# Optimization experiments

Hardware: AMD Instinct MI355X
Metric: run time of the kernel (lower is better)

Reference implementation:

```python
import jax, jax.numpy as jnp
import numpy as np

N = 100000   # nodes per node type ('net' and 'cell')
E = 600000   # edges per canonical relation
D_IN = 16    # raw input feature dim
D = 128      # hidden dim (in_size == out_size, required by wl: Linear(2*D -> D))
SLOPE = 0.2  # DGL GATConv leaky_relu negative slope


def setup_inputs() -> dict:
    key = jax.random.key(0)
    ks = jax.random.split(key, 24)
    f = lambda k, shp, scale=1.0: jax.random.normal(k, shp, dtype=jnp.float32) * scale
    s_in = 1.0 / np.sqrt(D_IN).astype(np.float32)
    s_d = 1.0 / np.sqrt(D).astype(np.float32)
    s_2d = 1.0 / np.sqrt(2 * D).astype(np.float32)
    inp = {
        'x_net':   f(ks[0], (N, D_IN)),
        'x_cell':  f(ks[1], (N, D_IN)),
        'Wp_net':  f(ks[2], (D, D_IN), s_in),
        'Wp_cell': f(ks[3], (D, D_IN), s_in),
        # per-edge-type GATConv params: fc weight + attn_l + attn_r (num_heads=1, no bias)
        'Wg0': f(ks[4], (D, D), s_d), 'al0': f(ks[5], (D,), s_d), 'ar0': f(ks[6], (D,), s_d),
        'Wg1': f(ks[7], (D, D), s_d), 'al1': f(ks[8], (D,), s_d), 'ar1': f(ks[9], (D,), s_d),
        'Wg2': f(ks[10], (D, D), s_d), 'al2': f(ks[11], (D,), s_d), 'ar2': f(ks[12], (D,), s_d),
        'Wl':   f(ks[13], (D, 2 * D), s_2d),
        'bias': jnp.zeros((D,), jnp.float32),
        # edge lists: relation 0 = cell->net, 1 = net->cell, 2 = net->net
        'src0': jax.random.randint(ks[14], (E,), 0, N, dtype=jnp.int32),
        'dst0': jax.random.randint(ks[15], (E,), 0, N, dtype=jnp.int32),
        'src1': jax.random.randint(ks[16], (E,), 0, N, dtype=jnp.int32),
        'dst1': jax.random.randint(ks[17], (E,), 0, N, dtype=jnp.int32),
        'src2': jax.random.randint(ks[18], (E,), 0, N, dtype=jnp.int32),
        'dst2': jax.random.randint(ks[19], (E,), 0, N, dtype=jnp.int32),
    }
    return inp


def _gat(x_src, x_dst, W, al, ar, src, dst):
    """DGL GATConv (num_heads=1, bias=False) on one relation's edge list."""
    h_src = x_src @ W.T                               # [N, D]
    h_dst = x_dst @ W.T                               # [N, D]
    el = (h_src @ al)[src]                            # [E] gathered src logits
    er = (h_dst @ ar)[dst]                            # [E] gathered dst logits
    e = jax.nn.leaky_relu(el + er, SLOPE)             # [E]
    # segment softmax over incoming edges of each dst node
    m = jax.ops.segment_max(e, dst, num_segments=N)
    ex = jnp.exp(e - m[dst])
    denom = jax.ops.segment_sum(ex, dst, num_segments=N)
    alpha = ex / denom[dst]                           # [E]
    return jax.ops.segment_sum(h_src[src] * alpha[:, None], dst, num_segments=N)


def reference(x_net, x_cell, Wp_net, Wp_cell,
              Wg0, al0, ar0, Wg1, al1, ar1, Wg2, al2, ar2,
              Wl, bias,
              src0, dst0, src1, dst1, src2, dst2):
    # feature projection per node type (ParaGraph.feat_proj)
    h_net = x_net @ Wp_net.T                          # [N, D]
    h_cell = x_cell @ Wp_cell.T                       # [N, D]
    feat = {'net': h_net, 'cell': h_cell}
    out = {'net': jnp.zeros((N, D), h_net.dtype), 'cell': jnp.zeros((N, D), h_cell.dtype)}
    # canonical etypes: (srctype, dsttype, gat params, edge list)
    rels = [
        ('cell', 'net', Wg0, al0, ar0, src0, dst0),
        ('net', 'cell', Wg1, al1, ar1, src1, dst1),
        ('net', 'net',  Wg2, al2, ar2, src2, dst2),
    ]
    for st, dt, W, al, ar, src, dst in rels:
        out[dt] = out[dt] + _gat(feat[st], feat[dt], W, al, ar, src, dst)
        # faithful to the original: concat+linear+relu recomputed for EVERY ntype
        # inside the etype loop (the redundant fused-op pattern)
        for nt in ('net', 'cell'):
            out[nt] = jax.nn.relu(
                jnp.concatenate([feat[nt], out[nt] + bias], axis=1) @ Wl.T)
    return jnp.stack([out['net'], out['cell']])      # [2, N, D]
```

## Files before the change

### kernel.cpp

```cpp
#include <hip/hip_runtime.h>
#include <hip/hip_bf16.h>
#include <stdint.h>

#define NN 100000
#define NE 600000
#define SP 136
#define NB 782
#define BCAP 1600
#define CHUNK 4096
#define NCH ((NE + CHUNK - 1) / CHUNK)

typedef unsigned short u16;
typedef unsigned int u32;
typedef __attribute__((ext_vector_type(8))) short short8;
typedef __attribute__((ext_vector_type(8))) __bf16 bf16x8;
typedef __attribute__((ext_vector_type(4))) float floatx4;

__device__ __forceinline__ float b2f(u16 u) {
  union { float f; u32 i; } c; c.i = ((u32)u) << 16; return c.f;
}
__device__ __forceinline__ u16 f2b(float f) {
  union { float f; u32 i; } c; c.f = f;
  u32 r = c.i + 0x7FFFu + ((c.i >> 16) & 1u);
  return (u16)(r >> 16);
}

__global__ __launch_bounds__(256) void conv_k(const float* __restrict__ Wl,
                                              const float* __restrict__ Wg0,
                                              const float* __restrict__ Wg1,
                                              const float* __restrict__ Wg2,
                                              u16* __restrict__ Wl_bf, u16* __restrict__ Wg_bf) {
  int y = blockIdx.y;
  const float* src = (y == 0) ? Wl : (y == 1) ? Wg0 : (y == 2) ? Wg1 : Wg2;
  u16* dst = (y == 0) ? Wl_bf : Wg_bf + (size_t)(y - 1) * 16384;
  int n = (y == 0) ? 32768 : 16384;
  int i = (blockIdx.x * 256 + threadIdx.x) * 4;
  if (i >= n) return;
  float4 v = *(const float4*)(src + i);
  ushort4 p; p.x = f2b(v.x); p.y = f2b(v.y); p.z = f2b(v.z); p.w = f2b(v.w);
  *(ushort4*)(dst + i) = p;
}

__global__ __launch_bounds__(256) void proj_k(const float* __restrict__ x_net, const float* __restrict__ x_cell,
                                              const float* __restrict__ Wp_net, const float* __restrict__ Wp_cell,
                                              u16* __restrict__ feat_net, u16* __restrict__ feat_cell) {
  const float* x  = blockIdx.y ? x_cell : x_net;
  const float* Wp = blockIdx.y ? Wp_cell : Wp_net;
  u16* feat       = blockIdx.y ? feat_cell : feat_net;
  __shared__ float Ws[128 * 17];
  __shared__ float xs[16][17];
  int tid = threadIdx.x;
#pragma unroll
  for (int it = 0; it < 8; ++it) {
    int idx = it * 256 + tid;
    int j = idx >> 4, k = idx & 15;
    Ws[j * 17 + k] = Wp[idx];
  }
  int n0 = blockIdx.x * 16;
  { int nn = tid >> 4, k = tid & 15;
    xs[nn][k] = x[(size_t)(n0 + nn) * 16 + k]; }
  __syncthreads();
  int j = tid & 127, g = tid >> 7;
  float acc[8];
#pragma unroll
  for (int r = 0; r < 8; ++r) acc[r] = 0.f;
#pragma unroll
  for (int k = 0; k < 16; ++k) {
    float w = Ws[j * 17 + k];
#pragma unroll
    for (int r = 0; r < 8; ++r) acc[r] += xs[g * 8 + r][k] * w;
  }
#pragma unroll
  for (int r = 0; r < 8; ++r)
    feat[(size_t)(n0 + g * 8 + r) * 128 + j] = f2b(acc[r]);
}

__global__ __launch_bounds__(128) void vec_k(const float* Wg0, const float* al0, const float* ar0,
                                             const float* Wg1, const float* al1, const float* ar1,
                                             const float* Wg2, const float* al2, const float* ar2,
                                             const float* Wl, const float* bias,
                                             float* __restrict__ vecs) {
  int a = blockIdx.x;
  int j = threadIdx.x;
  float s = 0.f;
  if (a < 6) {
    const float* W = (a < 2) ? Wg0 : (a < 4) ? Wg1 : Wg2;
    const float* v = (a == 0) ? al0 : (a == 1) ? ar0 : (a == 2) ? al1 : (a == 3) ? ar1 : (a == 4) ? al2 : ar2;
    for (int i = 0; i < 128; ++i) s += W[i * 128 + j] * v[i];
  } else {
    for (int i = 0; i < 128; ++i) s += Wl[(size_t)j * 256 + 128 + i] * bias[i];
  }
  vecs[a * 128 + j] = s;
}

__global__ __launch_bounds__(256) void logits_k(const u16* __restrict__ feat_net, const u16* __restrict__ feat_cell,
                                                const float* __restrict__ vecs, float* __restrict__ outs) {
  __shared__ float vs[6 * 128];
  int tid = threadIdx.x;
#pragma unroll
  for (int it = 0; it < 3; ++it) vs[it * 256 + tid] = vecs[it * 256 + tid];
  __syncthreads();
  int y = blockIdx.y;
  const u16* f = y ? feat_cell : feat_net;
  int n = blockIdx.x * 256 + tid;
  if (n >= NN) return;
  const u16* row = f + (size_t)n * 128;
  if (y == 0) {
    float s1 = 0.f, s2 = 0.f, s4 = 0.f, s5 = 0.f;
#pragma unroll
    for (int k = 0; k < 128; k += 8) {
      short8 u = *(const short8*)(row + k);
#pragma unroll
      for (int t = 0; t < 8; ++t) {
        float fv = b2f((u16)u[t]);
        s1 += fv * vs[1 * 128 + k + t]; s2 += fv * vs[2 * 128 + k + t];
        s4 += fv * vs[4 * 128 + k + t]; s5 += fv * vs[5 * 128 + k + t];
      }
    }
    outs[(size_t)1 * NN + n] = s1; outs[(size_t)2 * NN + n] = s2;
    outs[(size_t)4 * NN + n] = s4; outs[(size_t)5 * NN + n] = s5;
  } else {
    float s0 = 0.f, s3 = 0.f;
#pragma unroll
    for (int k = 0; k < 128; k += 8) {
      short8 u = *(const short8*)(row + k);
#pragma unroll
      for (int t = 0; t < 8; ++t) {
        float fv = b2f((u16)u[t]);
        s0 += fv * vs[0 * 128 + k + t]; s3 += fv * vs[3 * 128 + k + t];
      }
    }
    outs[(size_t)0 * NN + n] = s0; outs[(size_t)3 * NN + n] = s3;
  }
}

__global__ __launch_bounds__(256) void bhist_k(const int* __restrict__ dst0, const int* __restrict__ dst1,
                                               const int* __restrict__ dst2, int* __restrict__ bcnt) {
  int r = blockIdx.y;
  const int* dst = (r == 0) ? dst0 : (r == 1) ? dst1 : dst2;
  __shared__ int h[NB];
  int tid = threadIdx.x;
  for (int i = tid; i < NB; i += 256) h[i] = 0;
  __syncthreads();
  int e0 = blockIdx.x * CHUNK;
  int cnt = NE - e0; if (cnt > CHUNK) cnt = CHUNK;
  for (int i = tid; i < cnt; i += 256) atomicAdd(&h[((u32)dst[e0 + i]) >> 7], 1);
  __syncthreads();
  for (int b = tid; b < NB; b += 256) {
    int c = h[b];
    if (c) atomicAdd(&bcnt[(size_t)r * NB + b], c);
  }
}

__global__ __launch_bounds__(1024) void bscan_k(const int* __restrict__ bcnt, int* __restrict__ bptr,
                                                int* __restrict__ bcur) {
  int r = blockIdx.x, t = threadIdx.x;
  const int* c = bcnt + (size_t)r * NB;
  int* p = bptr + (size_t)r * (NB + 1);
  int* cur = bcur + (size_t)r * NB;
  int v = (t < NB) ? c[t] : 0;
  __shared__ int ss[1024];
  ss[t] = v; __syncthreads();
  for (int off = 1; off < 1024; off <<= 1) {
    int u = (t >= off) ? ss[t - off] : 0;
    __syncthreads();
    ss[t] += u;
    __syncthreads();
  }
  if (t < NB) { int e = ss[t] - v; p[t] = e; cur[t] = e; }
  if (t == 1023) p[NB] = ss[1023];
}

__global__ __launch_bounds__(256) void bscatter_k(const int* __restrict__ src0, const int* __restrict__ dst0,
                                                  const int* __restrict__ src1, const int* __restrict__ dst1,
                                                  const int* __restrict__ src2, const int* __restrict__ dst2,
                                                  int* __restrict__ bcur, u32* __restrict__ recs) {
  int r = blockIdx.y;
  const int* src = (r == 0) ? src0 : (r == 1) ? src1 : src2;
  const int* dst = (r == 0) ? dst0 : (r == 1) ? dst1 : dst2;
  __shared__ int hist[NB];
  __shared__ int lstart[NB];
  __shared__ int lcur[NB];
  __shared__ int badj[NB];
  __shared__ u32 rbuf[CHUNK];
  __shared__ u16 kbuf[CHUNK];
  __shared__ int ss[256];
  int tid = threadIdx.x;
  int e0 = blockIdx.x * CHUNK;
  int cnt = NE - e0; if (cnt > CHUNK) cnt = CHUNK;

  for (int i = tid; i < NB; i += 256) hist[i] = 0;
  __syncthreads();
  for (int i = tid; i < cnt; i += 256) atomicAdd(&hist[((u32)dst[e0 + i]) >> 7], 1);
  __syncthreads();
  int loc[4]; int s = 0;
  int base4 = tid * 4;
#pragma unroll
  for (int j = 0; j < 4; ++j) {
    int idx = base4 + j;
    int v = (idx < NB) ? hist[idx] : 0;
    loc[j] = s; s += v;
  }
  ss[tid] = s; __syncthreads();
  for (int off = 1; off < 256; off <<= 1) {
    int u = (tid >= off) ? ss[tid - off] : 0;
    __syncthreads();
    ss[tid] += u;
    __syncthreads();
  }
  int ex = ss[tid] - s;
#pragma unroll
  for (int j = 0; j < 4; ++j) {
    int idx = base4 + j;
    if (idx < NB) { int e = ex + loc[j]; lstart[idx] = e; lcur[idx] = e; }
  }
  __syncthreads();
  for (int b = tid; b < NB; b += 256) {
    int c = hist[b];
    int g = 0;
    if (c) g = atomicAdd(&bcur[(size_t)r * NB + b], c);
    badj[b] = g - lstart[b];
  }
  __syncthreads();
  for (int i = tid; i < cnt; i += 256) {
    int dN = dst[e0 + i], sN = src[e0 + i];
    int b = ((u32)dN) >> 7;
    int pos = atomicAdd(&lcur[b], 1);
    rbuf[pos] = ((u32)(dN & 127) << 17) | (u32)sN;
    kbuf[pos] = (u16)b;
  }
  __syncthreads();
  u32* out = recs + (size_t)r * NE;
  for (int i = tid; i < cnt; i += 256) {
    int b = kbuf[i];
    out[badj[b] + i] = rbuf[i];
  }
}

__global__ __launch_bounds__(256) void sort_k(u32* __restrict__ recs, const int* __restrict__ bptr,
                                              int* __restrict__ rowptr) {
  int r = blockIdx.y, b = blockIdx.x, tid = threadIdx.x;
  const int* p = bptr + (size_t)r * (NB + 1);
  u32* rec = recs + (size_t)r * NE;
  int* rp = rowptr + (size_t)r * (NN + 1);
  int base = p[b], end = p[b + 1];
  int cnt = end - base; if (cnt > BCAP) cnt = BCAP;
  __shared__ u32 rs[BCAP];
  __shared__ int hist[128], excl[128], cur[128];
  for (int i = tid; i < cnt; i += 256) rs[i] = rec[base + i];
  if (tid < 128) hist[tid] = 0;
  __syncthreads();
  for (int i = tid; i < cnt; i += 256) atomicAdd(&hist[rs[i] >> 17], 1);
  __syncthreads();
  if (tid < 128) cur[tid] = hist[tid];
  __syncthreads();
  for (int off = 1; off < 128; off <<= 1) {
    int v = 0;
    if (tid < 128 && tid >= off) v = cur[tid - off];
    __syncthreads();
    if (tid < 128) cur[tid] += v;
    __syncthreads();
  }
  if (tid < 128) {
    int e = cur[tid] - hist[tid];
    excl[tid] = e;
    int node = b * 128 + tid;
    if (node < NN) rp[node] = base + e;
  }
  if (b == NB - 1 && tid == 0) rp[NN] = p[NB];
  if (tid < 128) cur[tid] = excl[tid];
  __syncthreads();
  for (int i = tid; i < cnt; i += 256) {
    u32 v = rs[i];
    int pos = atomicAdd(&cur[v >> 17], 1);
    rec[base + pos] = v & 0x1FFFFu;
  }
}

template<int RMW>
__global__ __launch_bounds__(256) void agg_k(const u16* __restrict__ h, const u32* __restrict__ srecs,
                                             const int* __restrict__ rp,
                                             const float* __restrict__ el, const float* __restrict__ er,
                                             u16* __restrict__ out) {
  int tid = threadIdx.x;
  int sub = tid & 15;
  int n = blockIdx.x * 16 + (tid >> 4);
  int start = rp[n], end = rp[n + 1];
  u16* orow = out + (size_t)n * 128 + sub * 8;
  if (start == end) {
    if (!RMW) *(short8*)orow = short8{0, 0, 0, 0, 0, 0, 0, 0};
    return;
  }
  float ern = er[n];
  float acc[8];
#pragma unroll
  for (int t = 0; t < 8; ++t) acc[t] = 0.f;
  float sl = 0.f;
  const u16* hsub = h + sub * 8;
  for (int base = start; base < end; base += 16) {
    int m = end - base; if (m > 16) m = 16;
    int srci = 0; float w = 0.f;
    if (sub < m) {
      srci = (int)srecs[base + sub];
      float l = el[srci] + ern;
      l = (l >= 0.f) ? l : 0.2f * l;
      w = __expf(l);
    }
    sl += w;
    for (int i = 0; i < m; ++i) {
      float x = __shfl(w, i, 16);
      int sv = __shfl(srci, i, 16);
      short8 hv = *(const short8*)(hsub + (size_t)sv * 128);
#pragma unroll
      for (int t = 0; t < 8; ++t) acc[t] += x * b2f((u16)hv[t]);
    }
  }
  float s = sl;
#pragma unroll
  for (int off = 8; off > 0; off >>= 1) s += __shfl_xor(s, off, 16);
  float inv = 1.f / s;
  short8 o;
  if (RMW) {
    short8 pv = *(const short8*)orow;
#pragma unroll
    for (int t = 0; t < 8; ++t) o[t] = (short)f2b(b2f((u16)pv[t]) + acc[t] * inv);
  } else {
#pragma unroll
    for (int t = 0; t < 8; ++t) o[t] = (short)f2b(acc[t] * inv);
  }
  *(short8*)orow = o;
}

struct BJob { const u16* A; const u16* W; int ldw; int woff; u16* C; };
struct BJobs5 { BJob j[5]; };
__global__ __launch_bounds__(256) void gemm_bf_k(BJobs5 jobs) {
  BJob jb = jobs.j[blockIdx.y];
  __shared__ u16 Wlds[128 * SP];
  const int tid = threadIdx.x;
  const int row0 = blockIdx.x * 64;
#pragma unroll
  for (int it = 0; it < 8; ++it) {
    int idx = it * 256 + tid;
    int r = idx >> 4, c = (idx & 15) << 3;
    *(short8*)(&Wlds[r * SP + c]) = *(const short8*)(jb.W + (size_t)r * jb.ldw + jb.woff + c);
  }
  const int lane = tid & 63, wv = tid >> 6;
  const int m16 = lane & 15, quad = lane >> 4;
  int arow = row0 + wv * 16 + m16;
  if (arow >= NN) arow = NN - 1;
  const u16* Ab = jb.A + (size_t)arow * 128 + quad * 8;
  bf16x8 a[4];
#pragma unroll
  for (int kk = 0; kk < 4; ++kk) a[kk] = *(const bf16x8*)(Ab + kk * 32);
  __syncthreads();
  const u16* brow = &Wlds[m16 * SP + quad * 8];
  floatx4 acc[8];
#pragma unroll
  for (int c = 0; c < 8; ++c) acc[c] = floatx4{0.f, 0.f, 0.f, 0.f};
#pragma unroll
  for (int kk = 0; kk < 4; ++kk) {
#pragma unroll
    for (int c = 0; c < 8; ++c) {
      bf16x8 bfr = *(const bf16x8*)(brow + c * 16 * SP + kk * 32);
      acc[c] = __builtin_amdgcn_mfma_f32_16x16x32_bf16(a[kk], bfr, acc[c], 0, 0, 0);
    }
  }
#pragma unroll
  for (int c = 0; c < 8; ++c) {
    int col = c * 16 + m16;
#pragma unroll
    for (int r = 0; r < 4; ++r) {
      int grow = row0 + wv * 16 + quad * 4 + r;
      if (grow < NN) jb.C[(size_t)grow * 128 + col] = f2b(acc[c][r]);
    }
  }
}

struct FJob { const u16* A; const u16* P; void* C; };
struct FJobs2 { FJob j[2]; const u16* W; const float* cvec; };
template<int FINAL>
__global__ __launch_bounds__(256) void fused_k(FJobs2 jobs) {
  FJob jb = jobs.j[blockIdx.y];
  __shared__ u16 Wlds[128 * SP];
  const int tid = threadIdx.x;
  const int row0 = blockIdx.x * 64;
#pragma unroll
  for (int it = 0; it < 8; ++it) {
    int idx = it * 256 + tid;
    int r = idx >> 4, c = (idx & 15) << 3;
    *(short8*)(&Wlds[r * SP + c]) = *(const short8*)(jobs.W + (size_t)r * 256 + c);
  }
  const int lane = tid & 63, wv = tid >> 6;
  const int m16 = lane & 15, quad = lane >> 4;
  int arow = row0 + wv * 16 + m16;
  if (arow >= NN) arow = NN - 1;
  const u16* Ab = jb.A + (size_t)arow * 128 + quad * 8;
  bf16x8 a[4];
#pragma unroll
  for (int kk = 0; kk < 4; ++kk) a[kk] = *(const bf16x8*)(Ab + kk * 32);
  __syncthreads();
  const u16* brow = &Wlds[m16 * SP + quad * 8];
  floatx4 acc[8];
#pragma unroll
  for (int c = 0; c < 8; ++c) acc[c] = floatx4{0.f, 0.f, 0.f, 0.f};
#pragma unroll
  for (int kk = 0; kk < 4; ++kk) {
#pragma unroll
    for (int c = 0; c < 8; ++c) {
      bf16x8 bfr = *(const bf16x8*)(brow + c * 16 * SP + kk * 32);
      acc[c] = __builtin_amdgcn_mfma_f32_16x16x32_bf16(a[kk], bfr, acc[c], 0, 0, 0);
    }
  }
#pragma unroll
  for (int c = 0; c < 8; ++c) {
    int col = c * 16 + m16;
    float cv = jobs.cvec[col];
#pragma unroll
    for (int r = 0; r < 4; ++r) {
      int grow = row0 + wv * 16 + quad * 4 + r;
      if (grow < NN) {
        float v = acc[c][r] + b2f(jb.P[(size_t)grow * 128 + col]) + cv;
        v = fmaxf(v, 0.f);
        if (FINAL) ((float*)jb.C)[(size_t)grow * 128 + col] = v;
        else       ((u16*)jb.C)[(size_t)grow * 128 + col] = f2b(v);
      }
    }
  }
}

__global__ __launch_bounds__(256) void elem_k(const u16* __restrict__ P, const float* __restrict__ vecs,
                                              u16* __restrict__ out) {
  __shared__ float cs[128];
  if (threadIdx.x < 128) cs[threadIdx.x] = vecs[6 * 128 + threadIdx.x];
  __syncthreads();
  size_t idx = ((size_t)blockIdx.x * 256 + threadIdx.x) * 8;
  if (idx >= (size_t)NN * 128) return;
  int col = (int)(idx & 127);
  short8 u = *(const short8*)(P + idx);
  short8 w;
#pragma unroll
  for (int t = 0; t < 8; ++t)
    w[t] = (short)f2b(fmaxf(b2f((u16)u[t]) + cs[col + t], 0.f));
  *(short8*)(out + idx) = w;
}

extern "C" void kernel_launch(void* const* d_in, const int* in_sizes, int n_in,
                              void* d_out, int out_size, void* d_ws, size_t ws_size,
                              hipStream_t stream) {
  const float* x_net   = (const float*)d_in[0];
  const float* x_cell  = (const float*)d_in[1];
  const float* Wp_net  = (const float*)d_in[2];
  const float* Wp_cell = (const float*)d_in[3];
  const float* Wg[3] = {(const float*)d_in[4], (const float*)d_in[7], (const float*)d_in[10]};
  const float* al[3] = {(const float*)d_in[5], (const float*)d_in[8], (const float*)d_in[11]};
  const float* ar[3] = {(const float*)d_in[6], (const float*)d_in[9], (const float*)d_in[12]};
  const float* Wl    = (const float*)d_in[13];
  const float* bias  = (const float*)d_in[14];
  const int* src[3] = {(const int*)d_in[15], (const int*)d_in[17], (const int*)d_in[19]};
  const int* dst[3] = {(const int*)d_in[16], (const int*)d_in[18], (const int*)d_in[20]};

  char* ws = (char*)d_ws;
  size_t off = 0;
  auto alloc = [&](size_t b) { void* p = ws + off; off = (off + b + 255) & ~(size_t)255; return p; };
  u16*  feat_net  = (u16*)alloc((size_t)NN * 128 * 2);
  u16*  feat_cell = (u16*)alloc((size_t)NN * 128 * 2);
  u16*  hbuf0     = (u16*)alloc((size_t)NN * 128 * 2);
  u16*  hbuf1     = (u16*)alloc((size_t)NN * 128 * 2);
  u16*  hbuf2     = (u16*)alloc((size_t)NN * 128 * 2);
  u16*  P_net     = (u16*)alloc((size_t)NN * 128 * 2);
  u16*  P_cell    = (u16*)alloc((size_t)NN * 128 * 2);
  u16*  buf_net   = (u16*)alloc((size_t)NN * 128 * 2);
  u16*  buf_cell  = (u16*)alloc((size_t)NN * 128 * 2);
  float* vecs     = (float*)alloc(7 * 128 * 4);
  float* logit    = (float*)alloc((size_t)6 * NN * 4);
  u16*   Wl_bf    = (u16*)alloc((size_t)128 * 256 * 2);
  u16*   Wg_bf    = (u16*)alloc((size_t)3 * 128 * 128 * 2);
  int*   bcnt     = (int*)alloc((size_t)3 * NB * 4);
  int*   bcur     = (int*)alloc((size_t)3 * NB * 4);
  int*   bptr     = (int*)alloc((size_t)3 * (NB + 1) * 4);
  int*   rowptr   = (int*)alloc((size_t)3 * (NN + 1) * 4);
  u32*   recs     = (u32*)alloc((size_t)3 * NE * 4);

  hipMemsetAsync(bcnt, 0, (size_t)3 * NB * 4, stream);

  conv_k<<<dim3(32, 4), 256, 0, stream>>>(Wl, Wg[0], Wg[1], Wg[2], Wl_bf, Wg_bf);
  proj_k<<<dim3(NN / 16, 2), 256, 0, stream>>>(x_net, x_cell, Wp_net, Wp_cell, feat_net, feat_cell);
  vec_k<<<7, 128, 0, stream>>>(Wg[0], al[0], ar[0], Wg[1], al[1], ar[1], Wg[2], al[2], ar[2], Wl, bias, vecs);
  logits_k<<<dim3((NN + 255) / 256, 2), 256, 0, stream>>>(feat_net, feat_cell, vecs, logit);

  bhist_k<<<dim3(NCH, 3), 256, 0, stream>>>(dst[0], dst[1], dst[2], bcnt);
  bscan_k<<<3, 1024, 0, stream>>>(bcnt, bptr, bcur);
  bscatter_k<<<dim3(NCH, 3), 256, 0, stream>>>(src[0], dst[0], src[1], dst[1], src[2], dst[2],
                                               bcur, recs);
  sort_k<<<dim3(NB, 3), 256, 0, stream>>>(recs, bptr, rowptr);

  const int gb = (NN + 63) / 64;
  {
    BJobs5 jobs;
    jobs.j[0] = {feat_net,  Wl_bf,          256, 0, P_net};
    jobs.j[1] = {feat_cell, Wl_bf,          256, 0, P_cell};
    jobs.j[2] = {feat_cell, Wg_bf,          128, 0, hbuf0};
    jobs.j[3] = {feat_net,  Wg_bf + 16384,  128, 0, hbuf1};
    jobs.j[4] = {feat_net,  Wg_bf + 32768,  128, 0, hbuf2};
    gemm_bf_k<<<dim3(gb, 5), 256, 0, stream>>>(jobs);
  }

  float* out_f = (float*)d_out;
  const int ab = NN / 16;

  agg_k<0><<<ab, 256, 0, stream>>>(hbuf0, recs, rowptr, logit, logit + (size_t)NN, buf_net);
  {
    FJobs2 jobs; jobs.W = Wl_bf + 128; jobs.cvec = vecs + 6 * 128;
    jobs.j[0] = {buf_net, P_net, buf_net}; jobs.j[1] = jobs.j[0];
    fused_k<0><<<dim3(gb, 1), 256, 0, stream>>>(jobs);
  }
  elem_k<<<(NN * 128 / 8 + 255) / 256, 256, 0, stream>>>(P_cell, vecs, buf_cell);

  agg_k<1><<<ab, 256, 0, stream>>>(hbuf1, recs + (size_t)NE, rowptr + (NN + 1),
                                   logit + (size_t)2 * NN, logit + (size_t)3 * NN, buf_cell);
  {
    FJobs2 jobs; jobs.W = Wl_bf + 128; jobs.cvec = vecs + 6 * 128;
    jobs.j[0] = {buf_net, P_net, buf_net};
    jobs.j[1] = {buf_cell, P_cell, buf_cell};
    fused_k<0><<<dim3(gb, 2), 256, 0, stream>>>(jobs);
  }

  agg_k<1><<<ab, 256, 0, stream>>>(hbuf2, recs + (size_t)2 * NE, rowptr + 2 * (NN + 1),
                                   logit + (size_t)4 * NN, logit + (size_t)5 * NN, buf_net);
  {
    FJobs2 jobs; jobs.W = Wl_bf + 128; jobs.cvec = vecs + 6 * 128;
    jobs.j[0] = {buf_net, P_net, out_f};
    jobs.j[1] = {buf_cell, P_cell, out_f + (size_t)NN * 128};
    fused_k<1><<<dim3(gb, 2), 256, 0, stream>>>(jobs);
  }
}
```

Measured before the change: 517.9 us.

## Merge independent kernels into combined launches and reorder the per-relation stages

Several small or independent kernels are merged into multi-role launches that branch on block index: weight conversion, projection, vector precompute and zeroing of the histogram counts in one kernel; logits plus the bucket histogram in another; the sort plus the batched GEMM; and each aggregation paired with an independent fused linear job. The final cell output is computed alongside the last aggregation instead of after it. This cuts launch count and the idle tails between dependent stages by letting unrelated work fill the GPU together. In exchange the merged kernels take the larger shared-memory footprint of the GEMM role, which can lower occupancy for the aggregation blocks.

```diff
diff --git a/kernel.cpp b/kernel.cpp
--- a/kernel.cpp
+++ b/kernel.cpp
@@ -8,7 +8,9 @@
 #define NB 782
 #define BCAP 1600
 #define CHUNK 4096
-#define NCH ((NE + CHUNK - 1) / CHUNK)
+#define NCH 147
+#define GB 1563
+#define AB 6250
 
 typedef unsigned short u16;
 typedef unsigned int u32;
@@ -25,130 +27,274 @@
   return (u16)(r >> 16);
 }
 
-__global__ __launch_bounds__(256) void conv_k(const float* __restrict__ Wl,
-                                              const float* __restrict__ Wg0,
-                                              const float* __restrict__ Wg1,
-                                              const float* __restrict__ Wg2,
-                                              u16* __restrict__ Wl_bf, u16* __restrict__ Wg_bf) {
-  int y = blockIdx.y;
-  const float* src = (y == 0) ? Wl : (y == 1) ? Wg0 : (y == 2) ? Wg1 : Wg2;
-  u16* dst = (y == 0) ? Wl_bf : Wg_bf + (size_t)(y - 1) * 16384;
-  int n = (y == 0) ? 32768 : 16384;
-  int i = (blockIdx.x * 256 + threadIdx.x) * 4;
-  if (i >= n) return;
-  float4 v = *(const float4*)(src + i);
-  ushort4 p; p.x = f2b(v.x); p.y = f2b(v.y); p.z = f2b(v.z); p.w = f2b(v.w);
-  *(ushort4*)(dst + i) = p;
-}
-
-__global__ __launch_bounds__(256) void proj_k(const float* __restrict__ x_net, const float* __restrict__ x_cell,
-                                              const float* __restrict__ Wp_net, const float* __restrict__ Wp_cell,
-                                              u16* __restrict__ feat_net, u16* __restrict__ feat_cell) {
-  const float* x  = blockIdx.y ? x_cell : x_net;
-  const float* Wp = blockIdx.y ? Wp_cell : Wp_net;
-  u16* feat       = blockIdx.y ? feat_cell : feat_net;
-  __shared__ float Ws[128 * 17];
-  __shared__ float xs[16][17];
-  int tid = threadIdx.x;
+
+__device__ __forceinline__ void gemm_w(const u16* __restrict__ W, int ldw, u16* __restrict__ C,
+                                       u16* lds, int tid, int row0, const bf16x8* a,
+                                       int m16, int quad, int wv) {
 #pragma unroll
   for (int it = 0; it < 8; ++it) {
     int idx = it * 256 + tid;
-    int j = idx >> 4, k = idx & 15;
-    Ws[j * 17 + k] = Wp[idx];
-  }
-  int n0 = blockIdx.x * 16;
-  { int nn = tid >> 4, k = tid & 15;
-    xs[nn][k] = x[(size_t)(n0 + nn) * 16 + k]; }
-  __syncthreads();
-  int j = tid & 127, g = tid >> 7;
+    int r = idx >> 4, c = (idx & 15) << 3;
+    *(short8*)(&lds[r * SP + c]) = *(const short8*)(W + (size_t)r * ldw + c);
+  }
+  __syncthreads();
+  const u16* brow = &lds[m16 * SP + quad * 8];
+  floatx4 acc[8];
+#pragma unroll
+  for (int c = 0; c < 8; ++c) acc[c] = floatx4{0.f, 0.f, 0.f, 0.f};
+#pragma unroll
+  for (int kk = 0; kk < 4; ++kk) {
+#pragma unroll
+    for (int c = 0; c < 8; ++c) {
+      bf16x8 bfr = *(const bf16x8*)(brow + c * 16 * SP + kk * 32);
+      acc[c] = __builtin_amdgcn_mfma_f32_16x16x32_bf16(a[kk], bfr, acc[c], 0, 0, 0);
+    }
+  }
+#pragma unroll
+  for (int c = 0; c < 8; ++c) {
+    int col = c * 16 + m16;
+#pragma unroll
+    for (int r = 0; r < 4; ++r) {
+      int grow = row0 + wv * 16 + quad * 4 + r;
+      if (grow < NN) C[(size_t)grow * 128 + col] = f2b(acc[c][r]);
+    }
+  }
+}
+
+template<int FINAL>
+__device__ __forceinline__ void fused_body(int blk, int tid, const u16* __restrict__ A,
+                                           const u16* __restrict__ P, void* __restrict__ C,
+                                           const u16* __restrict__ W, const float* __restrict__ cvec,
+                                           u16* Wlds) {
+  const int row0 = blk * 64;
+#pragma unroll
+  for (int it = 0; it < 8; ++it) {
+    int idx = it * 256 + tid;
+    int r = idx >> 4, c = (idx & 15) << 3;
+    *(short8*)(&Wlds[r * SP + c]) = *(const short8*)(W + (size_t)r * 256 + c);
+  }
+  const int lane = tid & 63, wv = tid >> 6;
+  const int m16 = lane & 15, quad = lane >> 4;
+  int arow = row0 + wv * 16 + m16;
+  if (arow >= NN) arow = NN - 1;
+  const u16* Ab = A + (size_t)arow * 128 + quad * 8;
+  bf16x8 a[4];
+#pragma unroll
+  for (int kk = 0; kk < 4; ++kk) a[kk] = *(const bf16x8*)(Ab + kk * 32);
+  __syncthreads();
+  const u16* brow = &Wlds[m16 * SP + quad * 8];
+  floatx4 acc[8];
+#pragma unroll
+  for (int c = 0; c < 8; ++c) acc[c] = floatx4{0.f, 0.f, 0.f, 0.f};
+#pragma unroll
+  for (int kk = 0; kk < 4; ++kk) {
+#pragma unroll
+    for (int c = 0; c < 8; ++c) {
+      bf16x8 bfr = *(const bf16x8*)(brow + c * 16 * SP + kk * 32);
+      acc[c] = __builtin_amdgcn_mfma_f32_16x16x32_bf16(a[kk], bfr, acc[c], 0, 0, 0);
+    }
+  }
+#pragma unroll
+  for (int c = 0; c < 8; ++c) {
+    int col = c * 16 + m16;
+    float cv = cvec[col];
+#pragma unroll
+    for (int r = 0; r < 4; ++r) {
+      int grow = row0 + wv * 16 + quad * 4 + r;
+      if (grow < NN) {
+        float v = acc[c][r] + b2f(P[(size_t)grow * 128 + col]) + cv;
+        v = fmaxf(v, 0.f);
+        if (FINAL) ((float*)C)[(size_t)grow * 128 + col] = v;
+        else       ((u16*)C)[(size_t)grow * 128 + col] = f2b(v);
+      }
+    }
+  }
+}
+
+template<int RMW>
+__device__ __forceinline__ void agg_body(int nb, int tid, const u16* __restrict__ h,
+                                         const u32* __restrict__ srecs, const int* __restrict__ rp,
+                                         const float* __restrict__ el, const float* __restrict__ er,
+                                         u16* __restrict__ out) {
+  int sub = tid & 15;
+  int n = nb * 16 + (tid >> 4);
+  int start = rp[n], end = rp[n + 1];
+  u16* orow = out + (size_t)n * 128 + sub * 8;
+  if (start == end) {
+    if (!RMW) *(short8*)orow = short8{0, 0, 0, 0, 0, 0, 0, 0};
+    return;
+  }
+  float ern = er[n];
   float acc[8];
 #pragma unroll
-  for (int r = 0; r < 8; ++r) acc[r] = 0.f;
-#pragma unroll
-  for (int k = 0; k < 16; ++k) {
-    float w = Ws[j * 17 + k];
-#pragma unroll
-    for (int r = 0; r < 8; ++r) acc[r] += xs[g * 8 + r][k] * w;
-  }
-#pragma unroll
-  for (int r = 0; r < 8; ++r)
-    feat[(size_t)(n0 + g * 8 + r) * 128 + j] = f2b(acc[r]);
-}
-
-__global__ __launch_bounds__(128) void vec_k(const float* Wg0, const float* al0, const float* ar0,
-                                             const float* Wg1, const float* al1, const float* ar1,
-                                             const float* Wg2, const float* al2, const float* ar2,
-                                             const float* Wl, const float* bias,
-                                             float* __restrict__ vecs) {
-  int a = blockIdx.x;
-  int j = threadIdx.x;
-  float s = 0.f;
-  if (a < 6) {
-    const float* W = (a < 2) ? Wg0 : (a < 4) ? Wg1 : Wg2;
-    const float* v = (a == 0) ? al0 : (a == 1) ? ar0 : (a == 2) ? al1 : (a == 3) ? ar1 : (a == 4) ? al2 : ar2;
-    for (int i = 0; i < 128; ++i) s += W[i * 128 + j] * v[i];
+  for (int t = 0; t < 8; ++t) acc[t] = 0.f;
+  float sl = 0.f;
+  const u16* hsub = h + sub * 8;
+  for (int base = start; base < end; base += 16) {
+    int m = end - base; if (m > 16) m = 16;
+    int srci = 0; float w = 0.f;
+    if (sub < m) {
+      srci = (int)srecs[base + sub];
+      float l = el[srci] + ern;
+      l = (l >= 0.f) ? l : 0.2f * l;
+      w = __expf(l);
+    }
+    sl += w;
+    for (int i = 0; i < m; ++i) {
+      float x = __shfl(w, i, 16);
+      int sv = __shfl(srci, i, 16);
+      short8 hv = *(const short8*)(hsub + (size_t)sv * 128);
+#pragma unroll
+      for (int t = 0; t < 8; ++t) acc[t] += x * b2f((u16)hv[t]);
+    }
+  }
+  float s = sl;
+#pragma unroll
+  for (int off = 8; off > 0; off >>= 1) s += __shfl_xor(s, off, 16);
+  float inv = 1.f / s;
+  short8 o;
+  if (RMW) {
+    short8 pv = *(const short8*)orow;
+#pragma unroll
+    for (int t = 0; t < 8; ++t) o[t] = (short)f2b(b2f((u16)pv[t]) + acc[t] * inv);
   } else {
-    for (int i = 0; i < 128; ++i) s += Wl[(size_t)j * 256 + 128 + i] * bias[i];
-  }
-  vecs[a * 128 + j] = s;
-}
-
-__global__ __launch_bounds__(256) void logits_k(const u16* __restrict__ feat_net, const u16* __restrict__ feat_cell,
-                                                const float* __restrict__ vecs, float* __restrict__ outs) {
-  __shared__ float vs[6 * 128];
-  int tid = threadIdx.x;
-#pragma unroll
-  for (int it = 0; it < 3; ++it) vs[it * 256 + tid] = vecs[it * 256 + tid];
-  __syncthreads();
-  int y = blockIdx.y;
-  const u16* f = y ? feat_cell : feat_net;
-  int n = blockIdx.x * 256 + tid;
-  if (n >= NN) return;
-  const u16* row = f + (size_t)n * 128;
-  if (y == 0) {
-    float s1 = 0.f, s2 = 0.f, s4 = 0.f, s5 = 0.f;
-#pragma unroll
-    for (int k = 0; k < 128; k += 8) {
-      short8 u = *(const short8*)(row + k);
-#pragma unroll
-      for (int t = 0; t < 8; ++t) {
-        float fv = b2f((u16)u[t]);
-        s1 += fv * vs[1 * 128 + k + t]; s2 += fv * vs[2 * 128 + k + t];
-        s4 += fv * vs[4 * 128 + k + t]; s5 += fv * vs[5 * 128 + k + t];
+#pragma unroll
+    for (int t = 0; t < 8; ++t) o[t] = (short)f2b(acc[t] * inv);
+  }
+  *(short8*)orow = o;
+}
+
+
+__global__ __launch_bounds__(256) void prep_k(const float* __restrict__ x_net, const float* __restrict__ x_cell,
+                                              const float* __restrict__ Wp_net, const float* __restrict__ Wp_cell,
+                                              u16* __restrict__ feat_net, u16* __restrict__ feat_cell,
+                                              const float* __restrict__ Wl, const float* __restrict__ Wg0,
+                                              const float* __restrict__ Wg1, const float* __restrict__ Wg2,
+                                              u16* __restrict__ Wl_bf, u16* __restrict__ Wg_bf,
+                                              const float* al0, const float* ar0, const float* al1,
+                                              const float* ar1, const float* al2, const float* ar2,
+                                              const float* bias, float* __restrict__ vecs,
+                                              int* __restrict__ bcnt) {
+  int bid = blockIdx.x, tid = threadIdx.x;
+  if (bid < 2 * AB) {
+    int y = bid >= AB;
+    int bx = y ? bid - AB : bid;
+    const float* x  = y ? x_cell : x_net;
+    const float* Wp = y ? Wp_cell : Wp_net;
+    u16* feat       = y ? feat_cell : feat_net;
+    __shared__ float Ws[128 * 17];
+    __shared__ float xs[16][17];
+#pragma unroll
+    for (int it = 0; it < 8; ++it) {
+      int idx = it * 256 + tid;
+      int j = idx >> 4, k = idx & 15;
+      Ws[j * 17 + k] = Wp[idx];
+    }
+    int n0 = bx * 16;
+    { int nn = tid >> 4, k = tid & 15;
+      xs[nn][k] = x[(size_t)(n0 + nn) * 16 + k]; }
+    __syncthreads();
+    int j = tid & 127, g = tid >> 7;
+    float acc[8];
+#pragma unroll
+    for (int r = 0; r < 8; ++r) acc[r] = 0.f;
+#pragma unroll
+    for (int k = 0; k < 16; ++k) {
+      float w = Ws[j * 17 + k];
+#pragma unroll
+      for (int r = 0; r < 8; ++r) acc[r] += xs[g * 8 + r][k] * w;
+    }
+#pragma unroll
+    for (int r = 0; r < 8; ++r)
+      feat[(size_t)(n0 + g * 8 + r) * 128 + j] = f2b(acc[r]);
+  } else if (bid < 2 * AB + 128) {
+    int cid = bid - 2 * AB;
+    int y = cid >> 5, bx = cid & 31;
+    const float* src = (y == 0) ? Wl : (y == 1) ? Wg0 : (y == 2) ? Wg1 : Wg2;
+    u16* dst = (y == 0) ? Wl_bf : Wg_bf + (size_t)(y - 1) * 16384;
+    int n = (y == 0) ? 32768 : 16384;
+    int i = (bx * 256 + tid) * 4;
+    if (i >= n) return;
+    float4 v = *(const float4*)(src + i);
+    ushort4 p; p.x = f2b(v.x); p.y = f2b(v.y); p.z = f2b(v.z); p.w = f2b(v.w);
+    *(ushort4*)(dst + i) = p;
+  } else if (bid < 2 * AB + 135) {
+    int a = bid - (2 * AB + 128);
+    if (tid >= 128) return;
+    int j = tid;
+    float s = 0.f;
+    if (a < 6) {
+      const float* W = (a < 2) ? Wg0 : (a < 4) ? Wg1 : Wg2;
+      const float* v = (a == 0) ? al0 : (a == 1) ? ar0 : (a == 2) ? al1 : (a == 3) ? ar1 : (a == 4) ? al2 : ar2;
+      for (int i = 0; i < 128; ++i) s += W[i * 128 + j] * v[i];
+    } else {
+      for (int i = 0; i < 128; ++i) s += Wl[(size_t)j * 256 + 128 + i] * bias[i];
+    }
+    vecs[a * 128 + j] = s;
+  } else {
+    int r = bid - (2 * AB + 135);
+    for (int i = tid; i < NB; i += 256) bcnt[(size_t)r * NB + i] = 0;
+  }
+}
+
+__global__ __launch_bounds__(256) void logbh_k(const u16* __restrict__ feat_net, const u16* __restrict__ feat_cell,
+                                               const float* __restrict__ vecs, float* __restrict__ outs,
+                                               const int* __restrict__ dst0, const int* __restrict__ dst1,
+                                               const int* __restrict__ dst2, int* __restrict__ bcnt) {
+  __shared__ int sm[NB];
+  int bid = blockIdx.x, tid = threadIdx.x;
+  if (bid < 782) {
+    float* vs = (float*)sm;
+#pragma unroll
+    for (int it = 0; it < 3; ++it) vs[it * 256 + tid] = vecs[it * 256 + tid];
+    __syncthreads();
+    int y = bid >= 391;
+    int bx = y ? bid - 391 : bid;
+    const u16* f = y ? feat_cell : feat_net;
+    int n = bx * 256 + tid;
+    if (n >= NN) return;
+    const u16* row = f + (size_t)n * 128;
+    if (y == 0) {
+      float s1 = 0.f, s2 = 0.f, s4 = 0.f, s5 = 0.f;
+#pragma unroll
+      for (int k = 0; k < 128; k += 8) {
+        short8 u = *(const short8*)(row + k);
+#pragma unroll
+        for (int t = 0; t < 8; ++t) {
+          float fv = b2f((u16)u[t]);
+          s1 += fv * vs[1 * 128 + k + t]; s2 += fv * vs[2 * 128 + k + t];
+          s4 += fv * vs[4 * 128 + k + t]; s5 += fv * vs[5 * 128 + k + t];
+        }
       }
-    }
-    outs[(size_t)1 * NN + n] = s1; outs[(size_t)2 * NN + n] = s2;
-    outs[(size_t)4 * NN + n] = s4; outs[(size_t)5 * NN + n] = s5;
+      outs[(size_t)1 * NN + n] = s1; outs[(size_t)2 * NN + n] = s2;
+      outs[(size_t)4 * NN + n] = s4; outs[(size_t)5 * NN + n] = s5;
+    } else {
+      float s0 = 0.f, s3 = 0.f;
+#pragma unroll
+      for (int k = 0; k < 128; k += 8) {
+        short8 u = *(const short8*)(row + k);
+#pragma unroll
+        for (int t = 0; t < 8; ++t) {
+          float fv = b2f((u16)u[t]);
+          s0 += fv * vs[0 * 128 + k + t]; s3 += fv * vs[3 * 128 + k + t];
+        }
+      }
+      outs[(size_t)0 * NN + n] = s0; outs[(size_t)3 * NN + n] = s3;
+    }
   } else {
-    float s0 = 0.f, s3 = 0.f;
-#pragma unroll
-    for (int k = 0; k < 128; k += 8) {
-      short8 u = *(const short8*)(row + k);
-#pragma unroll
-      for (int t = 0; t < 8; ++t) {
-        float fv = b2f((u16)u[t]);
-        s0 += fv * vs[0 * 128 + k + t]; s3 += fv * vs[3 * 128 + k + t];
-      }
-    }
-    outs[(size_t)0 * NN + n] = s0; outs[(size_t)3 * NN + n] = s3;
-  }
-}
-
-__global__ __launch_bounds__(256) void bhist_k(const int* __restrict__ dst0, const int* __restrict__ dst1,
-                                               const int* __restrict__ dst2, int* __restrict__ bcnt) {
-  int r = blockIdx.y;
-  const int* dst = (r == 0) ? dst0 : (r == 1) ? dst1 : dst2;
-  __shared__ int h[NB];
-  int tid = threadIdx.x;
-  for (int i = tid; i < NB; i += 256) h[i] = 0;
-  __syncthreads();
-  int e0 = blockIdx.x * CHUNK;
-  int cnt = NE - e0; if (cnt > CHUNK) cnt = CHUNK;
-  for (int i = tid; i < cnt; i += 256) atomicAdd(&h[((u32)dst[e0 + i]) >> 7], 1);
-  __syncthreads();
-  for (int b = tid; b < NB; b += 256) {
-    int c = h[b];
-    if (c) atomicAdd(&bcnt[(size_t)r * NB + b], c);
+    int e = bid - 782;
+    int r = e / NCH, bx = e % NCH;
+    const int* dst = (r == 0) ? dst0 : (r == 1) ? dst1 : dst2;
+    for (int i = tid; i < NB; i += 256) sm[i] = 0;
+    __syncthreads();
+    int e0 = bx * CHUNK;
+    int cnt = NE - e0; if (cnt > CHUNK) cnt = CHUNK;
+    for (int i = tid; i < cnt; i += 256) atomicAdd(&sm[((u32)dst[e0 + i]) >> 7], 1);
+    __syncthreads();
+    for (int b = tid; b < NB; b += 256) {
+      int c = sm[b];
+      if (c) atomicAdd(&bcnt[(size_t)r * NB + b], c);
+    }
   }
 }
 
@@ -237,211 +383,141 @@
   }
 }
 
-__global__ __launch_bounds__(256) void sort_k(u32* __restrict__ recs, const int* __restrict__ bptr,
-                                              int* __restrict__ rowptr) {
-  int r = blockIdx.y, b = blockIdx.x, tid = threadIdx.x;
-  const int* p = bptr + (size_t)r * (NB + 1);
-  u32* rec = recs + (size_t)r * NE;
-  int* rp = rowptr + (size_t)r * (NN + 1);
-  int base = p[b], end = p[b + 1];
-  int cnt = end - base; if (cnt > BCAP) cnt = BCAP;
-  __shared__ u32 rs[BCAP];
-  __shared__ int hist[128], excl[128], cur[128];
-  for (int i = tid; i < cnt; i += 256) rs[i] = rec[base + i];
-  if (tid < 128) hist[tid] = 0;
-  __syncthreads();
-  for (int i = tid; i < cnt; i += 256) atomicAdd(&hist[rs[i] >> 17], 1);
-  __syncthreads();
-  if (tid < 128) cur[tid] = hist[tid];
-  __syncthreads();
-  for (int off = 1; off < 128; off <<= 1) {
-    int v = 0;
-    if (tid < 128 && tid >= off) v = cur[tid - off];
-    __syncthreads();
-    if (tid < 128) cur[tid] += v;
-    __syncthreads();
-  }
-  if (tid < 128) {
-    int e = cur[tid] - hist[tid];
-    excl[tid] = e;
-    int node = b * 128 + tid;
-    if (node < NN) rp[node] = base + e;
-  }
-  if (b == NB - 1 && tid == 0) rp[NN] = p[NB];
-  if (tid < 128) cur[tid] = excl[tid];
-  __syncthreads();
-  for (int i = tid; i < cnt; i += 256) {
-    u32 v = rs[i];
-    int pos = atomicAdd(&cur[v >> 17], 1);
-    rec[base + pos] = v & 0x1FFFFu;
-  }
-}
-
-template<int RMW>
-__global__ __launch_bounds__(256) void agg_k(const u16* __restrict__ h, const u32* __restrict__ srecs,
-                                             const int* __restrict__ rp,
-                                             const float* __restrict__ el, const float* __restrict__ er,
-                                             u16* __restrict__ out) {
-  int tid = threadIdx.x;
-  int sub = tid & 15;
-  int n = blockIdx.x * 16 + (tid >> 4);
-  int start = rp[n], end = rp[n + 1];
-  u16* orow = out + (size_t)n * 128 + sub * 8;
-  if (start == end) {
-    if (!RMW) *(short8*)orow = short8{0, 0, 0, 0, 0, 0, 0, 0};
-    return;
-  }
-  float ern = er[n];
-  float acc[8];
-#pragma unroll
-  for (int t = 0; t < 8; ++t) acc[t] = 0.f;
-  float sl = 0.f;
-  const u16* hsub = h + sub * 8;
-  for (int base = start; base < end; base += 16) {
-    int m = end - base; if (m > 16) m = 16;
-    int srci = 0; float w = 0.f;
-    if (sub < m) {
-      srci = (int)srecs[base + sub];
-      float l = el[srci] + ern;
-      l = (l >= 0.f) ? l : 0.2f * l;
-      w = __expf(l);
-    }
-    sl += w;
-    for (int i = 0; i < m; ++i) {
-      float x = __shfl(w, i, 16);
-      int sv = __shfl(srci, i, 16);
-      short8 hv = *(const short8*)(hsub + (size_t)sv * 128);
-#pragma unroll
-      for (int t = 0; t < 8; ++t) acc[t] += x * b2f((u16)hv[t]);
-    }
-  }
-  float s = sl;
-#pragma unroll
-  for (int off = 8; off > 0; off >>= 1) s += __shfl_xor(s, off, 16);
-  float inv = 1.f / s;
-  short8 o;
-  if (RMW) {
-    short8 pv = *(const short8*)orow;
-#pragma unroll
-    for (int t = 0; t < 8; ++t) o[t] = (short)f2b(b2f((u16)pv[t]) + acc[t] * inv);
+__global__ __launch_bounds__(256) void sortgemm_k(u32* __restrict__ recs, const int* __restrict__ bptr,
+                                                  int* __restrict__ rowptr,
+                                                  const u16* __restrict__ feat_net, const u16* __restrict__ feat_cell,
+                                                  const u16* __restrict__ Wl_bf, const u16* __restrict__ Wg_bf,
+                                                  u16* __restrict__ P_net, u16* __restrict__ P_cell,
+                                                  u16* __restrict__ h0, u16* __restrict__ h1, u16* __restrict__ h2) {
+  __shared__ u32 smem[128 * SP / 2];
+  int bid = blockIdx.x, tid = threadIdx.x;
+  if (bid < 3 * NB) {
+    int r = bid / NB, b = bid % NB;
+    const int* p = bptr + (size_t)r * (NB + 1);
+    u32* rec = recs + (size_t)r * NE;
+    int* rp = rowptr + (size_t)r * (NN + 1);
+    int base = p[b], end = p[b + 1];
+    int cnt = end - base; if (cnt > BCAP) cnt = BCAP;
+    u32* rs = smem;
+    int* hist = (int*)(smem + BCAP);
+    int* excl = hist + 128;
+    int* cur  = excl + 128;
+    for (int i = tid; i < cnt; i += 256) rs[i] = rec[base + i];
+    if (tid < 128) hist[tid] = 0;
+    __syncthreads();
+    for (int i = tid; i < cnt; i += 256) atomicAdd(&hist[rs[i] >> 17], 1);
+    __syncthreads();
+    if (tid < 128) cur[tid] = hist[tid];
+    __syncthreads();
+    for (int off = 1; off < 128; off <<= 1) {
+      int v = 0;
+      if (tid < 128 && tid >= off) v = cur[tid - off];
+      __syncthreads();
+      if (tid < 128) cur[tid] += v;
+      __syncthreads();
+    }
+    if (tid < 128) {
+      int e = cur[tid] - hist[tid];
+      excl[tid] = e;
+      int node = b * 128 + tid;
+      if (node < NN) rp[node] = base + e;
+    }
+    if (b == NB - 1 && tid == 0) rp[NN] = p[NB];
+    if (tid < 128) cur[tid] = excl[tid];
+    __syncthreads();
+    for (int i = tid; i < cnt; i += 256) {
+      u32 v = rs[i];
+      int pos = atomicAdd(&cur[v >> 17], 1);
+      rec[base + pos] = v & 0x1FFFFu;
+    }
   } else {
-#pragma unroll
-    for (int t = 0; t < 8; ++t) o[t] = (short)f2b(acc[t] * inv);
-  }
-  *(short8*)orow = o;
-}
-
-struct BJob { const u16* A; const u16* W; int ldw; int woff; u16* C; };
-struct BJobs5 { BJob j[5]; };
-__global__ __launch_bounds__(256) void gemm_bf_k(BJobs5 jobs) {
-  BJob jb = jobs.j[blockIdx.y];
+    int g = bid - 3 * NB;
+    int ntype = g >= GB;
+    int blk = ntype ? g - GB : g;
+    u16* lds = (u16*)smem;
+    const u16* A = ntype ? feat_cell : feat_net;
+    const int row0 = blk * 64;
+    const int lane = tid & 63, wv = tid >> 6;
+    const int m16 = lane & 15, quad = lane >> 4;
+    int arow = row0 + wv * 16 + m16;
+    if (arow >= NN) arow = NN - 1;
+    const u16* Ab = A + (size_t)arow * 128 + quad * 8;
+    bf16x8 a[4];
+#pragma unroll
+    for (int kk = 0; kk < 4; ++kk) a[kk] = *(const bf16x8*)(Ab + kk * 32);
+    if (!ntype) {
+      gemm_w(Wl_bf,          256, P_net, lds, tid, row0, a, m16, quad, wv);
+      __syncthreads();
+      gemm_w(Wg_bf + 16384,  128, h1,    lds, tid, row0, a, m16, quad, wv);
+      __syncthreads();
+      gemm_w(Wg_bf + 32768,  128, h2,    lds, tid, row0, a, m16, quad, wv);
+    } else {
+      gemm_w(Wl_bf,          256, P_cell, lds, tid, row0, a, m16, quad, wv);
+      __syncthreads();
+      gemm_w(Wg_bf,          128, h0,     lds, tid, row0, a, m16, quad, wv);
+    }
+  }
+}
+
+__global__ __launch_bounds__(256) void aggelem_k(const u16* __restrict__ h0, const u32* __restrict__ srecs,
+                                                 const int* __restrict__ rp,
+                                                 const float* __restrict__ el, const float* __restrict__ er,
+                                                 u16* __restrict__ buf_net,
+                                                 const u16* __restrict__ P_cell, const float* __restrict__ vecs,
+                                                 u16* __restrict__ buf_cell) {
+  int bid = blockIdx.x, tid = threadIdx.x;
+  if (bid < AB) {
+    agg_body<0>(bid, tid, h0, srecs, rp, el, er, buf_net);
+  } else {
+    __shared__ float cs[128];
+    int bx = bid - AB;
+    if (tid < 128) cs[tid] = vecs[6 * 128 + tid];
+    __syncthreads();
+    size_t idx = ((size_t)bx * 256 + tid) * 8;
+    if (idx >= (size_t)NN * 128) return;
+    int col = (int)(idx & 127);
+    short8 u = *(const short8*)(P_cell + idx);
+    short8 w;
+#pragma unroll
+    for (int t = 0; t < 8; ++t)
+      w[t] = (short)f2b(fmaxf(b2f((u16)u[t]) + cs[col + t], 0.f));
+    *(short8*)(buf_cell + idx) = w;
+  }
+}
+
+__global__ __launch_bounds__(256) void fusedagg_k(const u16* __restrict__ h1, const u32* __restrict__ srecs,
+                                                  const int* __restrict__ rp,
+                                                  const float* __restrict__ el, const float* __restrict__ er,
+                                                  u16* __restrict__ buf_cell,
+                                                  const u16* __restrict__ A, const u16* __restrict__ P_net,
+                                                  u16* __restrict__ Cnet,
+                                                  const u16* __restrict__ W, const float* __restrict__ cvec) {
   __shared__ u16 Wlds[128 * SP];
-  const int tid = threadIdx.x;
-  const int row0 = blockIdx.x * 64;
-#pragma unroll
-  for (int it = 0; it < 8; ++it) {
-    int idx = it * 256 + tid;
-    int r = idx >> 4, c = (idx & 15) << 3;
-    *(short8*)(&Wlds[r * SP + c]) = *(const short8*)(jb.W + (size_t)r * jb.ldw + jb.woff + c);
-  }
-  const int lane = tid & 63, wv = tid >> 6;
-  const int m16 = lane & 15, quad = lane >> 4;
-  int arow = row0 + wv * 16 + m16;
-  if (arow >= NN) arow = NN - 1;
-  const u16* Ab = jb.A + (size_t)arow * 128 + quad * 8;
-  bf16x8 a[4];
-#pragma unroll
-  for (int kk = 0; kk < 4; ++kk) a[kk] = *(const bf16x8*)(Ab + kk * 32);
-  __syncthreads();
-  const u16* brow = &Wlds[m16 * SP + quad * 8];
-  floatx4 acc[8];
-#pragma unroll
-  for (int c = 0; c < 8; ++c) acc[c] = floatx4{0.f, 0.f, 0.f, 0.f};
-#pragma unroll
-  for (int kk = 0; kk < 4; ++kk) {
-#pragma unroll
-    for (int c = 0; c < 8; ++c) {
-      bf16x8 bfr = *(const bf16x8*)(brow + c * 16 * SP + kk * 32);
-      acc[c] = __builtin_amdgcn_mfma_f32_16x16x32_bf16(a[kk], bfr, acc[c], 0, 0, 0);
-    }
-  }
-#pragma unroll
-  for (int c = 0; c < 8; ++c) {
-    int col = c * 16 + m16;
-#pragma unroll
-    for (int r = 0; r < 4; ++r) {
-      int grow = row0 + wv * 16 + quad * 4 + r;
-      if (grow < NN) jb.C[(size_t)grow * 128 + col] = f2b(acc[c][r]);
-    }
-  }
+  int bid = blockIdx.x, tid = threadIdx.x;
+  if (bid < AB) agg_body<1>(bid, tid, h1, srecs, rp, el, er, buf_cell);
+  else fused_body<0>(bid - AB, tid, A, P_net, (void*)Cnet, W, cvec, Wlds);
+}
+
+__global__ __launch_bounds__(256) void aggfused_k(const u16* __restrict__ h2, const u32* __restrict__ srecs,
+                                                  const int* __restrict__ rp,
+                                                  const float* __restrict__ el, const float* __restrict__ er,
+                                                  u16* __restrict__ buf_net,
+                                                  const u16* __restrict__ Acell, const u16* __restrict__ P_cell,
+                                                  float* __restrict__ Ccell,
+                                                  const u16* __restrict__ W, const float* __restrict__ cvec) {
+  __shared__ u16 Wlds[128 * SP];
+  int bid = blockIdx.x, tid = threadIdx.x;
+  if (bid < AB) agg_body<1>(bid, tid, h2, srecs, rp, el, er, buf_net);
+  else fused_body<1>(bid - AB, tid, Acell, P_cell, (void*)Ccell, W, cvec, Wlds);
 }
 
 struct FJob { const u16* A; const u16* P; void* C; };
 struct FJobs2 { FJob j[2]; const u16* W; const float* cvec; };
 template<int FINAL>
 __global__ __launch_bounds__(256) void fused_k(FJobs2 jobs) {
+  __shared__ u16 Wlds[128 * SP];
   FJob jb = jobs.j[blockIdx.y];
-  __shared__ u16 Wlds[128 * SP];
-  const int tid = threadIdx.x;
-  const int row0 = blockIdx.x * 64;
-#pragma unroll
-  for (int it = 0; it < 8; ++it) {
-    int idx = it * 256 + tid;
-    int r = idx >> 4, c = (idx & 15) << 3;
-    *(short8*)(&Wlds[r * SP + c]) = *(const short8*)(jobs.W + (size_t)r * 256 + c);
-  }
-  const int lane = tid & 63, wv = tid >> 6;
-  const int m16 = lane & 15, quad = lane >> 4;
-  int arow = row0 + wv * 16 + m16;
-  if (arow >= NN) arow = NN - 1;
-  const u16* Ab = jb.A + (size_t)arow * 128 + quad * 8;
-  bf16x8 a[4];
-#pragma unroll
-  for (int kk = 0; kk < 4; ++kk) a[kk] = *(const bf16x8*)(Ab + kk * 32);
-  __syncthreads();
-  const u16* brow = &Wlds[m16 * SP + quad * 8];
-  floatx4 acc[8];
-#pragma unroll
-  for (int c = 0; c < 8; ++c) acc[c] = floatx4{0.f, 0.f, 0.f, 0.f};
-#pragma unroll
-  for (int kk = 0; kk < 4; ++kk) {
-#pragma unroll
-    for (int c = 0; c < 8; ++c) {
-      bf16x8 bfr = *(const bf16x8*)(brow + c * 16 * SP + kk * 32);
-      acc[c] = __builtin_amdgcn_mfma_f32_16x16x32_bf16(a[kk], bfr, acc[c], 0, 0, 0);
-    }
-  }
-#pragma unroll
-  for (int c = 0; c < 8; ++c) {
-    int col = c * 16 + m16;
-    float cv = jobs.cvec[col];
-#pragma unroll
-    for (int r = 0; r < 4; ++r) {
-      int grow = row0 + wv * 16 + quad * 4 + r;
-      if (grow < NN) {
-        float v = acc[c][r] + b2f(jb.P[(size_t)grow * 128 + col]) + cv;
-        v = fmaxf(v, 0.f);
-        if (FINAL) ((float*)jb.C)[(size_t)grow * 128 + col] = v;
-        else       ((u16*)jb.C)[(size_t)grow * 128 + col] = f2b(v);
-      }
-    }
-  }
-}
-
-__global__ __launch_bounds__(256) void elem_k(const u16* __restrict__ P, const float* __restrict__ vecs,
-                                              u16* __restrict__ out) {
-  __shared__ float cs[128];
-  if (threadIdx.x < 128) cs[threadIdx.x] = vecs[6 * 128 + threadIdx.x];
-  __syncthreads();
-  size_t idx = ((size_t)blockIdx.x * 256 + threadIdx.x) * 8;
-  if (idx >= (size_t)NN * 128) return;
-  int col = (int)(idx & 127);
-  short8 u = *(const short8*)(P + idx);
-  short8 w;
-#pragma unroll
-  for (int t = 0; t < 8; ++t)
-    w[t] = (short)f2b(fmaxf(b2f((u16)u[t]) + cs[col + t], 0.f));
-  *(short8*)(out + idx) = w;
+  fused_body<FINAL>(blockIdx.x, threadIdx.x, jb.A, jb.P, jb.C, jobs.W, jobs.cvec, Wlds);
 }
 
 extern "C" void kernel_launch(void* const* d_in, const int* in_sizes, int n_in,
@@ -481,56 +557,37 @@
   int*   rowptr   = (int*)alloc((size_t)3 * (NN + 1) * 4);
   u32*   recs     = (u32*)alloc((size_t)3 * NE * 4);
 
-  hipMemsetAsync(bcnt, 0, (size_t)3 * NB * 4, stream);
-
-  conv_k<<<dim3(32, 4), 256, 0, stream>>>(Wl, Wg[0], Wg[1], Wg[2], Wl_bf, Wg_bf);
-  proj_k<<<dim3(NN / 16, 2), 256, 0, stream>>>(x_net, x_cell, Wp_net, Wp_cell, feat_net, feat_cell);
-  vec_k<<<7, 128, 0, stream>>>(Wg[0], al[0], ar[0], Wg[1], al[1], ar[1], Wg[2], al[2], ar[2], Wl, bias, vecs);
-  logits_k<<<dim3((NN + 255) / 256, 2), 256, 0, stream>>>(feat_net, feat_cell, vecs, logit);
-
-  bhist_k<<<dim3(NCH, 3), 256, 0, stream>>>(dst[0], dst[1], dst[2], bcnt);
+  float* out_f = (float*)d_out;
+
+  prep_k<<<2 * AB + 138, 256, 0, stream>>>(x_net, x_cell, Wp_net, Wp_cell, feat_net, feat_cell,
+                                           Wl, Wg[0], Wg[1], Wg[2], Wl_bf, Wg_bf,
+                                           al[0], ar[0], al[1], ar[1], al[2], ar[2], bias, vecs, bcnt);
+  logbh_k<<<782 + 3 * NCH, 256, 0, stream>>>(feat_net, feat_cell, vecs, logit,
+                                             dst[0], dst[1], dst[2], bcnt);
   bscan_k<<<3, 1024, 0, stream>>>(bcnt, bptr, bcur);
   bscatter_k<<<dim3(NCH, 3), 256, 0, stream>>>(src[0], dst[0], src[1], dst[1], src[2], dst[2],
                                                bcur, recs);
-  sort_k<<<dim3(NB, 3), 256, 0, stream>>>(recs, bptr, rowptr);
-
-  const int gb = (NN + 63) / 64;
-  {
-    BJobs5 jobs;
-    jobs.j[0] = {feat_net,  Wl_bf,          256, 0, P_net};
-    jobs.j[1] = {feat_cell, Wl_bf,          256, 0, P_cell};
-    jobs.j[2] = {feat_cell, Wg_bf,          128, 0, hbuf0};
-    jobs.j[3] = {feat_net,  Wg_bf + 16384,  128, 0, hbuf1};
-    jobs.j[4] = {feat_net,  Wg_bf + 32768,  128, 0, hbuf2};
-    gemm_bf_k<<<dim3(gb, 5), 256, 0, stream>>>(jobs);
-  }
-
-  float* out_f = (float*)d_out;
-  const int ab = NN / 16;
-
-  agg_k<0><<<ab, 256, 0, stream>>>(hbuf0, recs, rowptr, logit, logit + (size_t)NN, buf_net);
-  {
-    FJobs2 jobs; jobs.W = Wl_bf + 128; jobs.cvec = vecs + 6 * 128;
-    jobs.j[0] = {buf_net, P_net, buf_net}; jobs.j[1] = jobs.j[0];
-    fused_k<0><<<dim3(gb, 1), 256, 0, stream>>>(jobs);
-  }
-  elem_k<<<(NN * 128 / 8 + 255) / 256, 256, 0, stream>>>(P_cell, vecs, buf_cell);
-
-  agg_k<1><<<ab, 256, 0, stream>>>(hbuf1, recs + (size_t)NE, rowptr + (NN + 1),
-                                   logit + (size_t)2 * NN, logit + (size_t)3 * NN, buf_cell);
+  sortgemm_k<<<3 * NB + 2 * GB, 256, 0, stream>>>(recs, bptr, rowptr, feat_net, feat_cell,
+                                                  Wl_bf, Wg_bf, P_net, P_cell, hbuf0, hbuf1, hbuf2);
+  aggelem_k<<<2 * AB, 256, 0, stream>>>(hbuf0, recs, rowptr, logit, logit + (size_t)NN, buf_net,
+                                        P_cell, vecs, buf_cell);
+  fusedagg_k<<<AB + GB, 256, 0, stream>>>(hbuf1, recs + (size_t)NE, rowptr + (NN + 1),
+                                          logit + (size_t)2 * NN, logit + (size_t)3 * NN, buf_cell,
+                                          buf_net, P_net, buf_net, Wl_bf + 128, vecs + 6 * 128);
   {
     FJobs2 jobs; jobs.W = Wl_bf + 128; jobs.cvec = vecs + 6 * 128;
     jobs.j[0] = {buf_net, P_net, buf_net};
     jobs.j[1] = {buf_cell, P_cell, buf_cell};
-    fused_k<0><<<dim3(gb, 2), 256, 0, stream>>>(jobs);
-  }
-
-  agg_k<1><<<ab, 256, 0, stream>>>(hbuf2, recs + (size_t)2 * NE, rowptr + 2 * (NN + 1),
-                                   logit + (size_t)4 * NN, logit + (size_t)5 * NN, buf_net);
+    fused_k<0><<<dim3(GB, 2), 256, 0, stream>>>(jobs);
+  }
+  aggfused_k<<<AB + GB, 256, 0, stream>>>(hbuf2, recs + (size_t)2 * NE, rowptr + 2 * (NN + 1),
+                                          logit + (size_t)4 * NN, logit + (size_t)5 * NN, buf_net,
+                                          buf_cell, P_cell, out_f + (size_t)NN * 128,
+                                          Wl_bf + 128, vecs + 6 * 128);
   {
     FJobs2 jobs; jobs.W = Wl_bf + 128; jobs.cvec = vecs + 6 * 128;
     jobs.j[0] = {buf_net, P_net, out_f};
-    jobs.j[1] = {buf_cell, P_cell, out_f + (size_t)NN * 128};
-    fused_k<1><<<dim3(gb, 2), 256, 0, stream>>>(jobs);
-  }
-}
+    jobs.j[1] = jobs.j[0];
+    fused_k<1><<<dim3(GB, 1), 256, 0, stream>>>(jobs);
+  }
+}
```

Measured after the change: 503.5 us. -2.8%, faster.
